# Performance work log

Hardware: AMD Instinct MI355X
Metric: run time of the kernel (lower is better)

## Reference

```python
import jax, jax.numpy as jnp
import numpy as np

B, Z, DEG = 4096, 128, 16   # batch (dtPt), totalZONES, avg out-degree
E = Z * DEG                 # number of directed edges = number of tiny MLPs
WV = 0.1                    # WEIGHT_VARIANCE stand-in for normal_(0, WV) init


def setup_inputs() -> dict:
    key = jax.random.key(0)
    ks = jax.random.split(key, 7)
    x = jax.random.normal(ks[0], (B, Z), dtype=jnp.float32)
    # simple graph: each src zone has DEG distinct neighbors (no duplicate edges)
    rng = np.random.default_rng(0)
    dst = np.argsort(rng.random((Z, Z)), axis=1)[:, :DEG].reshape(-1)
    src = np.repeat(np.arange(Z), DEG)
    W1 = jax.random.normal(ks[1], (E, 2, 4), dtype=jnp.float32) * WV
    b1 = jax.random.normal(ks[2], (E, 4), dtype=jnp.float32) * WV
    W2 = jax.random.normal(ks[3], (E, 4, 4), dtype=jnp.float32) * WV
    b2 = jax.random.normal(ks[4], (E, 4), dtype=jnp.float32) * WV
    W3 = jax.random.normal(ks[5], (E, 4), dtype=jnp.float32) * WV  # Linear(4,1) weight, squeezed
    b3 = jax.random.normal(ks[6], (E,), dtype=jnp.float32) * WV
    return {"x": x, "dtPt": B,
            "src": jnp.asarray(src, jnp.int32), "dst": jnp.asarray(dst, jnp.int32),
            "W1": W1, "b1": b1, "W2": W2, "b2": b2, "W3": W3, "b3": b3}


def reference(x, dtPt, src, dst, W1, b1, W2, b2, W3, b3):
    # gather per-edge pair features: [B, E, 2]
    h = jnp.stack([x[:, src], x[:, dst]], axis=-1)
    # per-edge tiny MLP as batched GEMMs (one fused op over all E edges)
    h = jnp.tanh(jnp.einsum('bei,eio->beo', h, W1) + b1)   # [B, E, 4]
    h = jnp.tanh(jnp.einsum('bei,eio->beo', h, W2) + b2)   # [B, E, 4]
    beta = jax.nn.sigmoid(jnp.einsum('bei,ei->be', h, W3) + b3)  # [B, E]
    # scatter into ones-initialized adjacency output [B, Z, Z]
    out = jnp.ones((x.shape[0], Z, Z), dtype=x.dtype)
    return out.at[:, src, dst].set(beta)
```

## Files before the change

### kernel.cpp

```cpp
#include <hip/hip_runtime.h>


#define ZONES 128
#define NB    32

__device__ __forceinline__ float fast_tanh(float v) {
    float e = __expf(2.0f * v);
    return 1.0f - 2.0f * __builtin_amdgcn_rcpf(e + 1.0f);
}
__device__ __forceinline__ float fast_sigmoid(float v) {
    return __builtin_amdgcn_rcpf(1.0f + __expf(-v));
}

__global__ __launch_bounds__(256) void fused_edge_mlp(
    const float* __restrict__ x,
    const int*   __restrict__ dst,
    const float* __restrict__ W1,
    const float* __restrict__ b1,
    const float* __restrict__ W2,
    const float* __restrict__ b2,
    const float* __restrict__ W3,
    const float* __restrict__ b3,
    float* __restrict__ out)
{
    __shared__ float buf[2][2][8 * ZONES];

    const int tid  = threadIdx.x;
    const int rg   = blockIdx.x;
    const int b0   = blockIdx.y * NB;

    const int boff = tid >> 7;
    const int t    = tid & 127;
    const int e    = rg * 128 + t;
    const int srow = rg * 8 + (t >> 4);
    const int dcol = dst[e];

    float w1[8], b1v[4], w2[16], b2v[4], w3[4];
    *(float4*)&w1[0]  = ((const float4*)(W1 + e * 8))[0];
    *(float4*)&w1[4]  = ((const float4*)(W1 + e * 8))[1];
    *(float4*)&b1v[0] = ((const float4*)(b1 + e * 4))[0];
    *(float4*)&w2[0]  = ((const float4*)(W2 + e * 16))[0];
    *(float4*)&w2[4]  = ((const float4*)(W2 + e * 16))[1];
    *(float4*)&w2[8]  = ((const float4*)(W2 + e * 16))[2];
    *(float4*)&w2[12] = ((const float4*)(W2 + e * 16))[3];
    *(float4*)&b2v[0] = ((const float4*)(b2 + e * 4))[0];
    *(float4*)&w3[0]  = ((const float4*)(W3 + e * 4))[0];
    const float b3s = b3[e];

    float4* f4 = (float4*)buf;
    const float4 ones4 = make_float4(1.f, 1.f, 1.f, 1.f);
    #pragma unroll
    for (int i = 0; i < 4; ++i) f4[tid + 256 * i] = ones4;
    __syncthreads();

    float4* out4 = (float4*)out;
    const int scat = boff ? -1 : (t >> 4) * 128 + dcol;

    #pragma unroll 4
    for (int it = 0; it < NB / 2; ++it) {
        const int p = it & 1;
        const int b = b0 + it * 2 + boff;

        const float xs = x[b * ZONES + srow];
        const float xd = x[b * ZONES + dcol];

        float h1[4];
        #pragma unroll
        for (int o = 0; o < 4; ++o)
            h1[o] = fast_tanh(fmaf(xs, w1[o], fmaf(xd, w1[4 + o], b1v[o])));

        float h2[4];
        #pragma unroll
        for (int o = 0; o < 4; ++o) {
            float z = b2v[o];
            #pragma unroll
            for (int k = 0; k < 4; ++k)
                z = fmaf(h1[k], w2[k * 4 + o], z);
            h2[o] = fast_tanh(z);
        }

        float z = b3s;
        #pragma unroll
        for (int o = 0; o < 4; ++o)
            z = fmaf(h2[o], w3[o], z);
        const float beta = fast_sigmoid(z);

        buf[p][boff][(t >> 4) * 128 + dcol] = beta;
        __syncthreads();

        #pragma unroll
        for (int bb = 0; bb < 2; ++bb) {
            const int bw = b0 + it * 2 + bb;
            out4[(size_t)bw * (ZONES * ZONES / 4) + rg * 256 + tid] =
                ((float4*)buf[p][bb])[tid];
        }
    }
    (void)scat;
}

extern "C" void kernel_launch(void* const* d_in, const int* in_sizes, int n_in,
                              void* d_out, int out_size, void* d_ws, size_t ws_size,
                              hipStream_t stream) {
    const float* x   = (const float*)d_in[0];
    const int*   dst = (const int*)  d_in[3];
    const float* W1  = (const float*)d_in[4];
    const float* b1  = (const float*)d_in[5];
    const float* W2  = (const float*)d_in[6];
    const float* b2  = (const float*)d_in[7];
    const float* W3  = (const float*)d_in[8];
    const float* b3  = (const float*)d_in[9];
    float* out = (float*)d_out;

    const int B = in_sizes[0] / ZONES;
    dim3 grid(ZONES / 8, B / NB);
    fused_edge_mlp<<<grid, 256, 0, stream>>>(x, dst, W1, b1, W2, b2, W3, b3, out);
}
```

Before: 50.61 us.

## Replace LDS staging with direct ones-fill plus deferred global scatter of beta

Drops the shared-memory tile and per-iteration __syncthreads. Each wave now writes rows of ones straight to global memory and scatters the previous iteration's beta value into them after an explicit s_waitcnt, which keeps the writes ordered. Each block also covers twice as many batches. This removes block-wide barriers, but ordering now depends on vmcnt counting of same-thread stores and the scatter writes are uncoalesced.

```diff
diff --git a/kernel.cpp b/kernel.cpp
--- a/kernel.cpp
+++ b/kernel.cpp
@@ -2,7 +2,7 @@
 
 
 #define ZONES 128
-#define NB    32
+#define NB    64
 
 __device__ __forceinline__ float fast_tanh(float v) {
     float e = __expf(2.0f * v);
@@ -23,19 +23,21 @@
     const float* __restrict__ b3,
     float* __restrict__ out)
 {
-    __shared__ float buf[2][2][8 * ZONES];
-
     const int tid  = threadIdx.x;
+    const int w    = tid >> 6;
+    const int lane = tid & 63;
     const int rg   = blockIdx.x;
     const int b0   = blockIdx.y * NB;
 
-    const int boff = tid >> 7;
-    const int t    = tid & 127;
-    const int e    = rg * 128 + t;
-    const int srow = rg * 8 + (t >> 4);
+    const int boff = lane >> 5;
+    const int slot = lane & 31;
+    const int srow = rg * 8 + 2 * w + (slot >> 4);
+    const int e    = srow * 16 + (slot & 15);
     const int dcol = dst[e];
 
-    float w1[8], b1v[4], w2[16], b2v[4], w3[4];
+    const size_t obase = (size_t)((rg * 8 + 2 * w + boff) * 32 + slot);
+
+    float w1[8], b1v[4], w2[16], b2v[4], w3v[4];
     *(float4*)&w1[0]  = ((const float4*)(W1 + e * 8))[0];
     *(float4*)&w1[4]  = ((const float4*)(W1 + e * 8))[1];
     *(float4*)&b1v[0] = ((const float4*)(b1 + e * 4))[0];
@@ -44,25 +46,29 @@
     *(float4*)&w2[8]  = ((const float4*)(W2 + e * 16))[2];
     *(float4*)&w2[12] = ((const float4*)(W2 + e * 16))[3];
     *(float4*)&b2v[0] = ((const float4*)(b2 + e * 4))[0];
-    *(float4*)&w3[0]  = ((const float4*)(W3 + e * 4))[0];
+    *(float4*)&w3v[0] = ((const float4*)(W3 + e * 4))[0];
     const float b3s = b3[e];
 
-    float4* f4 = (float4*)buf;
+    float4* out4 = (float4*)out;
     const float4 ones4 = make_float4(1.f, 1.f, 1.f, 1.f);
-    #pragma unroll
-    for (int i = 0; i < 4; ++i) f4[tid + 256 * i] = ones4;
-    __syncthreads();
 
-    float4* out4 = (float4*)out;
-    const int scat = boff ? -1 : (t >> 4) * 128 + dcol;
+    float  pbeta = 0.f;
+    size_t paddr = 0;
 
     #pragma unroll 4
     for (int it = 0; it < NB / 2; ++it) {
-        const int p = it & 1;
-        const int b = b0 + it * 2 + boff;
+        const int bA = b0 + 2 * it;
+        const int bm = bA + boff;
 
-        const float xs = x[b * ZONES + srow];
-        const float xd = x[b * ZONES + dcol];
+        asm volatile("" ::: "memory");
+        const float xs = x[bm * ZONES + srow];
+        const float xd = x[bm * ZONES + dcol];
+        out4[(size_t)bA * 4096 + obase]       = ones4;
+        out4[(size_t)(bA + 1) * 4096 + obase] = ones4;
+        asm volatile("" ::: "memory");
+
+        asm volatile("s_waitcnt vmcnt(4)" ::: "memory");
+        if (it > 0) out[paddr] = pbeta;
 
         float h1[4];
         #pragma unroll
@@ -82,20 +88,14 @@
         float z = b3s;
         #pragma unroll
         for (int o = 0; o < 4; ++o)
-            z = fmaf(h2[o], w3[o], z);
-        const float beta = fast_sigmoid(z);
+            z = fmaf(h2[o], w3v[o], z);
 
-        buf[p][boff][(t >> 4) * 128 + dcol] = beta;
-        __syncthreads();
+        pbeta = fast_sigmoid(z);
+        paddr = (size_t)bm * (ZONES * ZONES) + srow * ZONES + dcol;
+    }
 
-        #pragma unroll
-        for (int bb = 0; bb < 2; ++bb) {
-            const int bw = b0 + it * 2 + bb;
-            out4[(size_t)bw * (ZONES * ZONES / 4) + rg * 256 + tid] =
-                ((float4*)buf[p][bb])[tid];
-        }
-    }
-    (void)scat;
+    asm volatile("s_waitcnt vmcnt(0)" ::: "memory");
+    out[paddr] = pbeta;
 }
 
 extern "C" void kernel_launch(void* const* d_in, const int* in_sizes, int n_in,
```

Result: slower. 97.18 us (+92.0%).
